# Kernel tuning notes

Measured on AMD Instinct MI355X. Metric: run time of the kernel, lower is better.

Reference implementation:

```python
import jax, jax.numpy as jnp
import numpy as np

N = 100000
E = 640000
D = 128
L = 3
B = 128
OUT = 10


def setup_inputs() -> dict:
    key = jax.random.key(0)
    ks = jax.random.split(key, 8)
    x = jax.random.normal(ks[0], (N, D), dtype=jnp.float32)
    edge_index = jax.random.randint(ks[1], (2, E), 0, N, dtype=jnp.int64)
    batch = jnp.sort(jax.random.randint(ks[2], (N,), 0, B, dtype=jnp.int64))
    # per-layer GCNConv weights (in==hidden==D so they stack) and biases
    Ws = jax.random.normal(ks[3], (L, D, D), dtype=jnp.float32) / np.sqrt(D)
    bs = jnp.zeros((L, D), dtype=jnp.float32)
    # MLP head: single Linear(hidden -> out), norm=None
    W_mlp = jax.random.normal(ks[4], (D, OUT), dtype=jnp.float32) / np.sqrt(D)
    b_mlp = jnp.zeros((OUT,), dtype=jnp.float32)
    return {"x": x, "edge_index": edge_index, "batch": batch,
            "Ws": Ws, "bs": bs, "W_mlp": W_mlp, "b_mlp": b_mlp}


def reference(x, edge_index, batch, Ws, bs, W_mlp, b_mlp):
    n = x.shape[0]
    # --- GCN normalization (PyG gcn_norm with self-loops, edge_weight=1) ---
    loop = jnp.arange(n, dtype=edge_index.dtype)
    src = jnp.concatenate([edge_index[0], loop])  # message sources (x_j)
    dst = jnp.concatenate([edge_index[1], loop])  # aggregation targets
    deg = jax.ops.segment_sum(jnp.ones_like(dst, dtype=x.dtype), dst, num_segments=n)
    dinv = jnp.where(deg > 0, jax.lax.rsqrt(jnp.maximum(deg, 1.0)), 0.0)
    norm = dinv[src] * dinv[dst]  # [E+N]

    def gcn_conv(h, W, b):
        hw = h @ W  # [N, D] dense transform
        msg = hw[src] * norm[:, None]  # gather + scale [E+N, D]
        agg = jax.ops.segment_sum(msg, dst, num_segments=n)  # scatter-add
        return agg + b

    h = x
    for l in range(Ws.shape[0]):
        h = jax.nn.relu(gcn_conv(h, Ws[l], bs[l]))

    # global add pool over graphs
    pooled = jax.ops.segment_sum(h, batch, num_segments=B)  # [B, D]
    # MLP head (single linear, no norm/act)
    return pooled @ W_mlp + b_mlp
```

## Files before the change

kernel.cpp:

```cpp
#include <hip/hip_runtime.h>
#include <hip/hip_bf16.h>

#define N_NODES 100000
#define N_EDGES 640000
#define DIM 128
#define N_LAYERS 3
#define N_GRAPHS 128
#define N_OUT 10
#define SCAN_BLK 1024
#define N_SCAN_BLKS ((N_NODES + SCAN_BLK - 1) / SCAN_BLK)
#define PCHUNK 128

typedef _Float16 h4 __attribute__((ext_vector_type(4)));
typedef _Float16 h2 __attribute__((ext_vector_type(2)));
typedef _Float16 h8 __attribute__((ext_vector_type(8)));
typedef float f32x4 __attribute__((ext_vector_type(4)));


__global__ void hist_dst(const int* __restrict__ ei, int* __restrict__ cnt) {
    int e = blockIdx.x * blockDim.x + threadIdx.x;
    if (e < N_EDGES) atomicAdd(&cnt[ei[N_EDGES + e]], 1);
}


__global__ void scan1(const int* __restrict__ cnt, int* __restrict__ off, int* __restrict__ bsum,
                      float* __restrict__ dinv) {
    __shared__ int tmp[256];
    int base = blockIdx.x * SCAN_BLK + threadIdx.x * 4;
    int c[4];
    #pragma unroll
    for (int k = 0; k < 4; ++k) c[k] = (base + k < N_NODES) ? cnt[base + k] : 0;
    #pragma unroll
    for (int k = 0; k < 4; ++k)
        if (base + k < N_NODES) dinv[base + k] = rsqrtf((float)(c[k] + 1));
    int tot = c[0] + c[1] + c[2] + c[3];
    tmp[threadIdx.x] = tot;
    __syncthreads();
    int val = tot;
    for (int d = 1; d < 256; d <<= 1) {
        int add = (threadIdx.x >= d) ? tmp[threadIdx.x - d] : 0;
        __syncthreads();
        val += add;
        tmp[threadIdx.x] = val;
        __syncthreads();
    }
    int ex = val - tot;
    int e1 = ex + c[0], e2 = e1 + c[1], e3 = e2 + c[2];
    if (base + 0 < N_NODES) off[base + 0] = ex;
    if (base + 1 < N_NODES) off[base + 1] = e1;
    if (base + 2 < N_NODES) off[base + 2] = e2;
    if (base + 3 < N_NODES) off[base + 3] = e3;
    if (threadIdx.x == 255) bsum[blockIdx.x] = val;
}

__global__ void scan2(int* __restrict__ bsum) {
    __shared__ int tmp[128];
    int t = threadIdx.x;
    int v = (t < N_SCAN_BLKS) ? bsum[t] : 0;
    int own = v;
    tmp[t] = v;
    __syncthreads();
    for (int d = 1; d < 128; d <<= 1) {
        int add = (t >= d) ? tmp[t - d] : 0;
        __syncthreads();
        v += add;
        tmp[t] = v;
        __syncthreads();
    }
    if (t < N_SCAN_BLKS) bsum[t] = v - own;
}

__global__ void scan3(int* __restrict__ off, const int* __restrict__ bsum) {
    int i = blockIdx.x * blockDim.x + threadIdx.x;
    if (i < N_NODES) off[i] += bsum[i / SCAN_BLK];
    if (i == 0) off[N_NODES] = N_EDGES;
}


__global__ void fill_csr(const int* __restrict__ ei, const int* __restrict__ off,
                         int* __restrict__ cursor, int* __restrict__ csr_src) {
    int e = blockIdx.x * blockDim.x + threadIdx.x;
    if (e >= N_EDGES) return;
    int s = ei[e], d = ei[N_EDGES + e];
    int pos = off[d] + atomicAdd(&cursor[d], 1);
    csr_src[pos] = s;
}


__global__ void wt_prep(const float* __restrict__ Ws, _Float16* __restrict__ wt) {
    int t = blockIdx.x * blockDim.x + threadIdx.x;
    if (t >= N_LAYERS * DIM * 32) return;
    int u = t & 31;
    int n = (t >> 5) & 127;
    int l = t >> 12;
    const float* W = Ws + (size_t)l * DIM * DIM;
    int k0 = u * 4;
    h4 v;
    v.x = (_Float16)W[(k0 + 0) * DIM + n];
    v.y = (_Float16)W[(k0 + 1) * DIM + n];
    v.z = (_Float16)W[(k0 + 2) * DIM + n];
    v.w = (_Float16)W[(k0 + 3) * DIM + n];
    int du = u ^ (n & 31);
    ((h4*)wt)[(size_t)l * 4096 + n * 32 + du] = v;
}


__device__ __forceinline__ h4 loadfrag(const _Float16* p) { return *(const h4*)p; }
__device__ __forceinline__ h4 loadfrag(const float* p) {
    float4 f = *(const float4*)p;
    h4 v; v.x = (_Float16)f.x; v.y = (_Float16)f.y; v.z = (_Float16)f.z; v.w = (_Float16)f.w;
    return v;
}

template<typename TIN>
__global__ __launch_bounds__(256) void gemm_mfma(const TIN* __restrict__ in,
                                                 const _Float16* __restrict__ wt,
                                                 const float* __restrict__ dinv,
                                                 _Float16* __restrict__ out) {
    __shared__ h4 Wl[4096];
    {
        const float4* src = (const float4*)wt;
        float4* dst = (float4*)Wl;
        #pragma unroll
        for (int i = 0; i < 8; ++i) dst[threadIdx.x + i * 256] = src[threadIdx.x + i * 256];
    }
    __syncthreads();

    const int wave = threadIdx.x >> 6;
    const int lane = threadIdx.x & 63;
    const int m0 = blockIdx.x * 64 + wave * 16;
    if (m0 >= N_NODES) return;

    const int row = lane & 15;
    const int g   = lane >> 4;
    const int m   = m0 + row;
    const TIN* arow = in + (size_t)m * DIM;
    const float di = dinv[m];

    f32x4 acc[8] = {};

    #pragma unroll
    for (int kc = 0; kc < 8; ++kc) {
        const int k = kc * 16 + g * 4;
        const h4 bfrag = loadfrag(arow + k);
        const int u = kc * 4 + g;
        #pragma unroll
        for (int nb = 0; nb < 8; ++nb) {
            const int n = nb * 16 + row;
            const h4 afrag = Wl[n * 32 + (u ^ (n & 31))];
            acc[nb] = __builtin_amdgcn_mfma_f32_16x16x16f16(afrag, bfrag, acc[nb], 0, 0, 0);
        }
    }

    _Float16* orow = out + (size_t)m * DIM;
    #pragma unroll
    for (int nb = 0; nb < 8; ++nb) {
        h4 v;
        v.x = (_Float16)(acc[nb].x * di); v.y = (_Float16)(acc[nb].y * di);
        v.z = (_Float16)(acc[nb].z * di); v.w = (_Float16)(acc[nb].w * di);
        ((h4*)orow)[nb * 4 + g] = v;
    }
}


__global__ __launch_bounds__(256) void gather_agg(const _Float16* __restrict__ hw,
                                                  const float* __restrict__ dinv,
                                                  const int* __restrict__ off,
                                                  const int* __restrict__ csr_src,
                                                  const float* __restrict__ bias,
                                                  _Float16* __restrict__ hout) {
    const int i = (blockIdx.x * blockDim.x + threadIdx.x) >> 6;
    if (i >= N_NODES) return;
    const int lane = threadIdx.x & 63;
    const int grp    = lane >> 3;
    const int stream = grp & 3;
    const int half   = grp >> 2;
    const int sub    = lane & 7;
    const int idx8   = half * 8 + sub;
    const h8* hw8 = (const h8*)hw;

    const int beg = off[i], end = off[i + 1];
    h8 acc = {};

    if (stream == 3) acc = hw8[(size_t)i * 16 + idx8];

    int j = beg + stream;
    for (; j + 4 < end; j += 8) {
        int s0 = csr_src[j];
        int s1 = csr_src[j + 4];
        h8 v0 = hw8[(size_t)s0 * 16 + idx8];
        h8 v1 = hw8[(size_t)s1 * 16 + idx8];
        #pragma unroll
        for (int p = 0; p < 4; ++p) {
            ((h2*)&acc)[p] += ((h2*)&v0)[p];
            ((h2*)&acc)[p] += ((h2*)&v1)[p];
        }
    }
    for (; j < end; j += 4) {
        int s0 = csr_src[j];
        h8 v0 = hw8[(size_t)s0 * 16 + idx8];
        #pragma unroll
        for (int p = 0; p < 4; ++p) ((h2*)&acc)[p] += ((h2*)&v0)[p];
    }

    unsigned int* au = (unsigned int*)&acc;
    #pragma unroll
    for (int p = 0; p < 4; ++p) {
        unsigned int o = __shfl_xor(au[p], 8);
        h2 a = *(h2*)&au[p]; a += *(h2*)&o; au[p] = *(unsigned int*)&a;
        o = __shfl_xor(au[p], 16);
        h2 b = *(h2*)&au[p]; b += *(h2*)&o; au[p] = *(unsigned int*)&b;
    }

    if (stream == 0) {
        const float di = dinv[i];
        const float4 b0 = *(const float4*)&bias[half * 64 + sub * 8];
        const float4 b1 = *(const float4*)&bias[half * 64 + sub * 8 + 4];
        h8 v;
        v[0] = (_Float16)fmaxf((float)acc[0] * di + b0.x, 0.0f);
        v[1] = (_Float16)fmaxf((float)acc[1] * di + b0.y, 0.0f);
        v[2] = (_Float16)fmaxf((float)acc[2] * di + b0.z, 0.0f);
        v[3] = (_Float16)fmaxf((float)acc[3] * di + b0.w, 0.0f);
        v[4] = (_Float16)fmaxf((float)acc[4] * di + b1.x, 0.0f);
        v[5] = (_Float16)fmaxf((float)acc[5] * di + b1.y, 0.0f);
        v[6] = (_Float16)fmaxf((float)acc[6] * di + b1.z, 0.0f);
        v[7] = (_Float16)fmaxf((float)acc[7] * di + b1.w, 0.0f);
        ((h8*)hout)[(size_t)i * 16 + idx8] = v;
    }
}


__global__ __launch_bounds__(256) void pool_chunk(const _Float16* __restrict__ h,
                                                  const int* __restrict__ batch,
                                                  float* __restrict__ pooled) {
    const int base = blockIdx.x * PCHUNK;
    const int t = threadIdx.x;
    const int lane4 = t & 31;
    const int rgrp = t >> 5;
    const h4* hp = (const h4*)h;

    float a0 = 0.f, a1 = 0.f, a2 = 0.f, a3 = 0.f;
    int cur = -1;
    const int rend = (base + PCHUNK < N_NODES) ? base + PCHUNK : N_NODES;
    for (int r = base + rgrp; r < rend; r += 8) {
        int b = batch[r];
        if (b != cur) {
            if (cur >= 0) {
                float* pp = &pooled[cur * DIM + lane4 * 4];
                atomicAdd(pp + 0, a0); atomicAdd(pp + 1, a1);
                atomicAdd(pp + 2, a2); atomicAdd(pp + 3, a3);
            }
            cur = b; a0 = a1 = a2 = a3 = 0.f;
        }
        h4 v = hp[(size_t)r * 32 + lane4];
        a0 += (float)v.x; a1 += (float)v.y; a2 += (float)v.z; a3 += (float)v.w;
    }
    if (cur >= 0) {
        float* pp = &pooled[cur * DIM + lane4 * 4];
        atomicAdd(pp + 0, a0); atomicAdd(pp + 1, a1);
        atomicAdd(pp + 2, a2); atomicAdd(pp + 3, a3);
    }
}


__global__ void mlp_head(const float* __restrict__ pooled, const float* __restrict__ Wm,
                         const float* __restrict__ bm, float* __restrict__ out) {
    int t = blockIdx.x * blockDim.x + threadIdx.x;
    if (t >= N_GRAPHS * N_OUT) return;
    int b = t / N_OUT;
    int o = t % N_OUT;
    float acc = bm[o];
    #pragma unroll 8
    for (int k = 0; k < DIM; ++k) acc += pooled[b * DIM + k] * Wm[k * N_OUT + o];
    out[t] = acc;
}


extern "C" void kernel_launch(void* const* d_in, const int* in_sizes, int n_in,
                              void* d_out, int out_size, void* d_ws, size_t ws_size,
                              hipStream_t stream) {
    const float* x     = (const float*)d_in[0];
    const int*   ei    = (const int*)d_in[1];
    const int*   batch = (const int*)d_in[2];
    const float* Ws    = (const float*)d_in[3];
    const float* bs    = (const float*)d_in[4];
    const float* Wm    = (const float*)d_in[5];
    const float* bm    = (const float*)d_in[6];
    float* out = (float*)d_out;

    char* p = (char*)d_ws;
    int*      cnt     = (int*)p;        p += N_NODES * 4;
    int*      cursor  = (int*)p;        p += N_NODES * 4;
    float*    dinv    = (float*)p;      p += N_NODES * 4;
    int*      csr_off = (int*)p;        p += (N_NODES + 16) * 4;
    int*      bsum    = (int*)p;        p += 128 * 4;
    _Float16* wt      = (_Float16*)p;   p += (size_t)N_LAYERS * DIM * DIM * 2;
    int*      csr_src = (int*)p;        p += (size_t)N_EDGES * 4;
    _Float16* bufA    = (_Float16*)p;   p += (size_t)N_NODES * DIM * 2;
    _Float16* bufB    = (_Float16*)p;   p += (size_t)N_NODES * DIM * 2;
    float*    pooled  = (float*)p;      p += N_GRAPHS * DIM * 4;

    const int nnode_blk = (N_NODES + 255) / 256;
    const int nedge_blk = (N_EDGES + 255) / 256;

    hipMemsetAsync(cnt, 0, N_NODES * 8, stream);
    hipMemsetAsync(pooled, 0, N_GRAPHS * DIM * 4, stream);

    hist_dst<<<nedge_blk, 256, 0, stream>>>(ei, cnt);
    wt_prep<<<(N_LAYERS * DIM * 32 + 255) / 256, 256, 0, stream>>>(Ws, wt);

    scan1<<<N_SCAN_BLKS, 256, 0, stream>>>(cnt, csr_off, bsum, dinv);
    scan2<<<1, 128, 0, stream>>>(bsum);
    scan3<<<nnode_blk, 256, 0, stream>>>(csr_off, bsum);

    fill_csr<<<nedge_blk, 256, 0, stream>>>(ei, csr_off, cursor, csr_src);

    const int gemm_grid = (N_NODES + 63) / 64;
    const int gather_grid = (N_NODES * 64 + 255) / 256;
    for (int l = 0; l < N_LAYERS; ++l) {
        if (l == 0) gemm_mfma<float><<<gemm_grid, 256, 0, stream>>>(x, wt, dinv, bufA);
        else        gemm_mfma<_Float16><<<gemm_grid, 256, 0, stream>>>(bufB, wt + (size_t)l * DIM * DIM, dinv, bufA);
        gather_agg<<<gather_grid, 256, 0, stream>>>(bufA, dinv, csr_off, csr_src, bs + l * DIM, bufB);
    }

    pool_chunk<<<(N_NODES + PCHUNK - 1) / PCHUNK, 256, 0, stream>>>(bufB, batch, pooled);
    mlp_head<<<(N_GRAPHS * N_OUT + 255) / 256, 256, 0, stream>>>(pooled, Wm, bm, out);
}
```

Measured before the change: 301.4 us.

## Partition edge atomics by XCD node range and make GEMM persistent

The histogram and CSR fill kernels now launch 256 blocks. Each block scans one edge slice and handles only the destinations in the node range that belongs to its XCD group, chosen as blockIdx mod 8. This is meant to keep each node's atomics within one XCD's L2 and avoid cross-die atomic traffic. The cost is that every edge is read eight times, and fewer threads run in total. The GEMM switches to a grid-stride persistent loop over 512 blocks, so the weight copy into LDS is paid once per block rather than once per 64 rows.

```diff
diff --git a/kernel.cpp b/kernel.cpp
--- a/kernel.cpp
+++ b/kernel.cpp
@@ -10,6 +10,10 @@
 #define SCAN_BLK 1024
 #define N_SCAN_BLKS ((N_NODES + SCAN_BLK - 1) / SCAN_BLK)
 #define PCHUNK 128
+#define NXCD 8
+#define RNODES (N_NODES / NXCD)
+#define ESLICES 32
+#define ESLICE (N_EDGES / ESLICES)
 
 typedef _Float16 h4 __attribute__((ext_vector_type(4)));
 typedef _Float16 h2 __attribute__((ext_vector_type(2)));
@@ -17,9 +21,15 @@
 typedef float f32x4 __attribute__((ext_vector_type(4)));
 
 
-__global__ void hist_dst(const int* __restrict__ ei, int* __restrict__ cnt) {
-    int e = blockIdx.x * blockDim.x + threadIdx.x;
-    if (e < N_EDGES) atomicAdd(&cnt[ei[N_EDGES + e]], 1);
+__global__ __launch_bounds__(256) void hist_dst(const int* __restrict__ ei, int* __restrict__ cnt) {
+    const int g = blockIdx.x & (NXCD - 1);
+    const int b = blockIdx.x >> 3;
+    const int lo = g * RNODES, hi = lo + RNODES;
+    const int e0 = b * ESLICE;
+    for (int e = e0 + threadIdx.x; e < e0 + ESLICE; e += 256) {
+        int d = ei[N_EDGES + e];
+        if (d >= lo && d < hi) atomicAdd(&cnt[d], 1);
+    }
 }
 
 
@@ -77,13 +87,20 @@
 }
 
 
-__global__ void fill_csr(const int* __restrict__ ei, const int* __restrict__ off,
-                         int* __restrict__ cursor, int* __restrict__ csr_src) {
-    int e = blockIdx.x * blockDim.x + threadIdx.x;
-    if (e >= N_EDGES) return;
-    int s = ei[e], d = ei[N_EDGES + e];
-    int pos = off[d] + atomicAdd(&cursor[d], 1);
-    csr_src[pos] = s;
+__global__ __launch_bounds__(256) void fill_csr(const int* __restrict__ ei, const int* __restrict__ off,
+                                                int* __restrict__ cursor, int* __restrict__ csr_src) {
+    const int g = blockIdx.x & (NXCD - 1);
+    const int b = blockIdx.x >> 3;
+    const int lo = g * RNODES, hi = lo + RNODES;
+    const int e0 = b * ESLICE;
+    for (int e = e0 + threadIdx.x; e < e0 + ESLICE; e += 256) {
+        int d = ei[N_EDGES + e];
+        if (d >= lo && d < hi) {
+            int s = ei[e];
+            int pos = off[d] + atomicAdd(&cursor[d], 1);
+            csr_src[pos] = s;
+        }
+    }
 }
 
 
@@ -128,37 +145,39 @@
 
     const int wave = threadIdx.x >> 6;
     const int lane = threadIdx.x & 63;
-    const int m0 = blockIdx.x * 64 + wave * 16;
-    if (m0 >= N_NODES) return;
-
     const int row = lane & 15;
     const int g   = lane >> 4;
-    const int m   = m0 + row;
-    const TIN* arow = in + (size_t)m * DIM;
-    const float di = dinv[m];
-
-    f32x4 acc[8] = {};
-
-    #pragma unroll
-    for (int kc = 0; kc < 8; ++kc) {
-        const int k = kc * 16 + g * 4;
-        const h4 bfrag = loadfrag(arow + k);
-        const int u = kc * 4 + g;
+
+    for (int c0 = blockIdx.x * 64; c0 < N_NODES; c0 += gridDim.x * 64) {
+        const int m0 = c0 + wave * 16;
+        if (m0 >= N_NODES) continue;
+        const int m = m0 + row;
+        const TIN* arow = in + (size_t)m * DIM;
+        const float di = dinv[m];
+
+        f32x4 acc[8] = {};
+
+        #pragma unroll
+        for (int kc = 0; kc < 8; ++kc) {
+            const int k = kc * 16 + g * 4;
+            const h4 bfrag = loadfrag(arow + k);
+            const int u = kc * 4 + g;
+            #pragma unroll
+            for (int nb = 0; nb < 8; ++nb) {
+                const int n = nb * 16 + row;
+                const h4 afrag = Wl[n * 32 + (u ^ (n & 31))];
+                acc[nb] = __builtin_amdgcn_mfma_f32_16x16x16f16(afrag, bfrag, acc[nb], 0, 0, 0);
+            }
+        }
+
+        _Float16* orow = out + (size_t)m * DIM;
         #pragma unroll
         for (int nb = 0; nb < 8; ++nb) {
-            const int n = nb * 16 + row;
-            const h4 afrag = Wl[n * 32 + (u ^ (n & 31))];
-            acc[nb] = __builtin_amdgcn_mfma_f32_16x16x16f16(afrag, bfrag, acc[nb], 0, 0, 0);
-        }
-    }
-
-    _Float16* orow = out + (size_t)m * DIM;
-    #pragma unroll
-    for (int nb = 0; nb < 8; ++nb) {
-        h4 v;
-        v.x = (_Float16)(acc[nb].x * di); v.y = (_Float16)(acc[nb].y * di);
-        v.z = (_Float16)(acc[nb].z * di); v.w = (_Float16)(acc[nb].w * di);
-        ((h4*)orow)[nb * 4 + g] = v;
+            h4 v;
+            v.x = (_Float16)(acc[nb].x * di); v.y = (_Float16)(acc[nb].y * di);
+            v.z = (_Float16)(acc[nb].z * di); v.w = (_Float16)(acc[nb].w * di);
+            ((h4*)orow)[nb * 4 + g] = v;
+        }
     }
 }
 
@@ -301,21 +320,20 @@
     float*    pooled  = (float*)p;      p += N_GRAPHS * DIM * 4;
 
     const int nnode_blk = (N_NODES + 255) / 256;
-    const int nedge_blk = (N_EDGES + 255) / 256;
 
     hipMemsetAsync(cnt, 0, N_NODES * 8, stream);
     hipMemsetAsync(pooled, 0, N_GRAPHS * DIM * 4, stream);
 
-    hist_dst<<<nedge_blk, 256, 0, stream>>>(ei, cnt);
+    hist_dst<<<NXCD * ESLICES, 256, 0, stream>>>(ei, cnt);
     wt_prep<<<(N_LAYERS * DIM * 32 + 255) / 256, 256, 0, stream>>>(Ws, wt);
 
     scan1<<<N_SCAN_BLKS, 256, 0, stream>>>(cnt, csr_off, bsum, dinv);
     scan2<<<1, 128, 0, stream>>>(bsum);
     scan3<<<nnode_blk, 256, 0, stream>>>(csr_off, bsum);
 
-    fill_csr<<<nedge_blk, 256, 0, stream>>>(ei, csr_off, cursor, csr_src);
-
-    const int gemm_grid = (N_NODES + 63) / 64;
+    fill_csr<<<NXCD * ESLICES, 256, 0, stream>>>(ei, csr_off, cursor, csr_src);
+
+    const int gemm_grid = 512;
     const int gather_grid = (N_NODES * 64 + 255) / 256;
     for (int l = 0; l < N_LAYERS; ++l) {
         if (l == 0) gemm_mfma<float><<<gemm_grid, 256, 0, stream>>>(x, wt, dinv, bufA);
```

New measurement: 326.5 us. 8.3% more time.

## Bucket edges by destination range and pin atomics per XCD

Applied to the files above, without the earlier changes.

Adds a pre-pass that partitions edges into 8 destination-node ranges in a staging buffer. The histogram and CSR-fill kernels then run with blockIdx mod 8 selecting the range, assuming round-robin block-to-XCD dispatch. The goal is to keep each XCD's atomics on cnt and cursor local to its own L2 slice and avoid cross-XCD atomic contention. This costs an extra kernel, an 8-byte-per-edge staging write and read, and a fixed 98304-entry per-range capacity that holds only for roughly uniform destinations.

```diff
diff --git a/kernel.cpp b/kernel.cpp
--- a/kernel.cpp
+++ b/kernel.cpp
@@ -10,6 +10,11 @@
 #define SCAN_BLK 1024
 #define N_SCAN_BLKS ((N_NODES + SCAN_BLK - 1) / SCAN_BLK)
 #define PCHUNK 128
+#define NXCD 8
+#define RNODES (N_NODES / NXCD)
+#define R_EST 98304
+#define BE 1000
+#define RK 40
 
 typedef _Float16 h4 __attribute__((ext_vector_type(4)));
 typedef _Float16 h2 __attribute__((ext_vector_type(2)));
@@ -17,9 +22,51 @@
 typedef float f32x4 __attribute__((ext_vector_type(4)));
 
 
-__global__ void hist_dst(const int* __restrict__ ei, int* __restrict__ cnt) {
-    int e = blockIdx.x * blockDim.x + threadIdx.x;
-    if (e < N_EDGES) atomicAdd(&cnt[ei[N_EDGES + e]], 1);
+__global__ __launch_bounds__(256) void bucket_edges(const int* __restrict__ ei,
+                                                    int* __restrict__ rangeCur,
+                                                    int2* __restrict__ staging) {
+    __shared__ int hist[NXCD];
+    __shared__ int base[NXCD];
+    const int e0 = blockIdx.x * BE;
+    if (threadIdx.x < NXCD) hist[threadIdx.x] = 0;
+    __syncthreads();
+
+    int s[4], d[4], r[4];
+    #pragma unroll
+    for (int k = 0; k < 4; ++k) {
+        int e = e0 + threadIdx.x + k * 256;
+        if (e < e0 + BE) {
+            s[k] = ei[e];
+            d[k] = ei[N_EDGES + e];
+            r[k] = d[k] / RNODES;
+            atomicAdd(&hist[r[k]], 1);
+        } else r[k] = -1;
+    }
+    __syncthreads();
+    if (threadIdx.x < NXCD) base[threadIdx.x] = atomicAdd(&rangeCur[threadIdx.x], hist[threadIdx.x]);
+    __syncthreads();
+    if (threadIdx.x < NXCD) hist[threadIdx.x] = 0;
+    __syncthreads();
+
+    #pragma unroll
+    for (int k = 0; k < 4; ++k) {
+        if (r[k] >= 0) {
+            int idx = base[r[k]] + atomicAdd(&hist[r[k]], 1);
+            staging[(size_t)r[k] * R_EST + idx] = make_int2(s[k], d[k]);
+        }
+    }
+}
+
+
+__global__ __launch_bounds__(256) void hist_pinned(const int2* __restrict__ staging,
+                                                   const int* __restrict__ rangeCur,
+                                                   int* __restrict__ cnt) {
+    const int g = blockIdx.x & (NXCD - 1);
+    const int b = blockIdx.x >> 3;
+    const int n = rangeCur[g];
+    const int2* st = staging + (size_t)g * R_EST;
+    for (int j = b * 256 + threadIdx.x; j < n; j += RK * 256)
+        atomicAdd(&cnt[st[j].y], 1);
 }
 
 
@@ -77,13 +124,20 @@
 }
 
 
-__global__ void fill_csr(const int* __restrict__ ei, const int* __restrict__ off,
-                         int* __restrict__ cursor, int* __restrict__ csr_src) {
-    int e = blockIdx.x * blockDim.x + threadIdx.x;
-    if (e >= N_EDGES) return;
-    int s = ei[e], d = ei[N_EDGES + e];
-    int pos = off[d] + atomicAdd(&cursor[d], 1);
-    csr_src[pos] = s;
+__global__ __launch_bounds__(256) void fill_pinned(const int2* __restrict__ staging,
+                                                   const int* __restrict__ rangeCur,
+                                                   const int* __restrict__ off,
+                                                   int* __restrict__ cursor,
+                                                   int* __restrict__ csr_src) {
+    const int g = blockIdx.x & (NXCD - 1);
+    const int b = blockIdx.x >> 3;
+    const int n = rangeCur[g];
+    const int2* st = staging + (size_t)g * R_EST;
+    for (int j = b * 256 + threadIdx.x; j < n; j += RK * 256) {
+        int2 sd = st[j];
+        int pos = off[sd.y] + atomicAdd(&cursor[sd.y], 1);
+        csr_src[pos] = sd.x;
+    }
 }
 
 
@@ -289,31 +343,34 @@
     float* out = (float*)d_out;
 
     char* p = (char*)d_ws;
-    int*      cnt     = (int*)p;        p += N_NODES * 4;
-    int*      cursor  = (int*)p;        p += N_NODES * 4;
-    float*    dinv    = (float*)p;      p += N_NODES * 4;
-    int*      csr_off = (int*)p;        p += (N_NODES + 16) * 4;
-    int*      bsum    = (int*)p;        p += 128 * 4;
-    _Float16* wt      = (_Float16*)p;   p += (size_t)N_LAYERS * DIM * DIM * 2;
-    int*      csr_src = (int*)p;        p += (size_t)N_EDGES * 4;
-    _Float16* bufA    = (_Float16*)p;   p += (size_t)N_NODES * DIM * 2;
-    _Float16* bufB    = (_Float16*)p;   p += (size_t)N_NODES * DIM * 2;
-    float*    pooled  = (float*)p;      p += N_GRAPHS * DIM * 4;
+    int*      cnt      = (int*)p;        p += N_NODES * 4;
+    int*      cursor   = (int*)p;        p += N_NODES * 4;
+    int*      rangeCur = (int*)p;        p += 16 * 4;
+    float*    dinv     = (float*)p;      p += N_NODES * 4;
+    int*      csr_off  = (int*)p;        p += (N_NODES + 16) * 4;
+    int*      bsum     = (int*)p;        p += 128 * 4;
+    _Float16* wt       = (_Float16*)p;   p += (size_t)N_LAYERS * DIM * DIM * 2;
+    int*      csr_src  = (int*)p;        p += (size_t)N_EDGES * 4;
+    int2*     staging  = (int2*)p;       p += (size_t)NXCD * R_EST * 8;
+    _Float16* bufA     = (_Float16*)p;   p += (size_t)N_NODES * DIM * 2;
+    _Float16* bufB     = (_Float16*)p;   p += (size_t)N_NODES * DIM * 2;
+    float*    pooled   = (float*)p;      p += N_GRAPHS * DIM * 4;
 
     const int nnode_blk = (N_NODES + 255) / 256;
-    const int nedge_blk = (N_EDGES + 255) / 256;
-
-    hipMemsetAsync(cnt, 0, N_NODES * 8, stream);
+
+    hipMemsetAsync(cnt, 0, N_NODES * 8 + 16 * 4, stream);
     hipMemsetAsync(pooled, 0, N_GRAPHS * DIM * 4, stream);
 
-    hist_dst<<<nedge_blk, 256, 0, stream>>>(ei, cnt);
+    bucket_edges<<<N_EDGES / BE, 256, 0, stream>>>(ei, rangeCur, staging);
     wt_prep<<<(N_LAYERS * DIM * 32 + 255) / 256, 256, 0, stream>>>(Ws, wt);
+
+    hist_pinned<<<NXCD * RK, 256, 0, stream>>>(staging, rangeCur, cnt);
 
     scan1<<<N_SCAN_BLKS, 256, 0, stream>>>(cnt, csr_off, bsum, dinv);
     scan2<<<1, 128, 0, stream>>>(bsum);
     scan3<<<nnode_blk, 256, 0, stream>>>(csr_off, bsum);
 
-    fill_csr<<<nedge_blk, 256, 0, stream>>>(ei, csr_off, cursor, csr_src);
+    fill_pinned<<<NXCD * RK, 256, 0, stream>>>(staging, rangeCur, csr_off, cursor, csr_src);
 
     const int gemm_grid = (N_NODES + 63) / 64;
     const int gather_grid = (N_NODES * 64 + 255) / 256;
```

Result: faster. 290.2 us (-3.7%).
